# Kernel tuning notes

Hardware: AMD Instinct MI355X
Metric: run time of the kernel (lower is better)

Reference implementation:

```python
import jax, jax.numpy as jnp
import numpy as np

ENCODER_STRIDE = 320
TEMPERATURE = 1.0


def setup_inputs() -> dict:
    key = jax.random.key(0)
    k1, k2, k3, k4 = jax.random.split(key, 4)
    B, D, T, K = 8, 512, 4096, 4096
    student_features = jax.random.normal(k1, (B, D, T), dtype=jnp.float32)
    codebook = jax.random.normal(k2, (K, D), dtype=jnp.float32)
    teacher_codes = jax.random.randint(k3, (B, T), 0, K, dtype=jnp.int64)
    lengths = jax.random.randint(k4, (B,), 0, T * ENCODER_STRIDE, dtype=jnp.int64)
    return {
        "student_features": student_features,
        "codebook": codebook,
        "teacher_codes": teacher_codes,
        "lengths": lengths,
    }


def reference(student_features, codebook, teacher_codes, lengths):
    B, D, T = student_features.shape
    # length mask over frames: frame t is valid if its start sample < length
    frame_starts = jnp.arange(T, dtype=jnp.int64) * ENCODER_STRIDE  # [T]
    mask = (frame_starts[None, :] < lengths[:, None]).astype(student_features.dtype)  # [B,T]

    z = jnp.transpose(student_features, (0, 2, 1)).reshape(-1, D)  # [N,D], N=B*T

    # cdist p=2: sqrt(|z|^2 + |c|^2 - 2 z.c)
    z2 = jnp.sum(z * z, axis=1, keepdims=True)            # [N,1]
    c2 = jnp.sum(codebook * codebook, axis=1)[None, :]    # [1,K]
    d2 = z2 + c2 - 2.0 * (z @ codebook.T)                 # [N,K]
    dists = jnp.sqrt(jnp.maximum(d2, 1e-12))

    soft_weights = jax.nn.softmax(-dists / TEMPERATURE, axis=1)  # [N,K]
    soft_recon = soft_weights @ codebook                          # [N,D]

    codes_flat = teacher_codes.reshape(-1)                        # [N]
    target_embeddings = jax.lax.stop_gradient(codebook[codes_flat])  # [N,D]

    diff_sq = jnp.mean((soft_recon - target_embeddings) ** 2, axis=1).reshape(B, T)
    loss = jnp.sum(diff_sq * mask) / (jnp.sum(mask) + 1e-8)
    return loss
```

## Files before the change

### kernel.cpp

```cpp
#include <hip/hip_runtime.h>
#include <hip/hip_bf16.h>


#define BB 8
#define DD 512
#define TT 4096
#define KKK 4096
#define ENC_STRIDE 320
#define KT 32
#define NKT (KKK / KT)
#define NW 8
#define ROWS 128
#define KBROW 2056
#define KBBYTES 4112
#define BUFB (8 * KBBYTES)

typedef __attribute__((ext_vector_type(8))) short bf16x8;
typedef __attribute__((ext_vector_type(4))) float f32x4;

union FragU { bf16x8 v; uint2 h2[2]; ushort us[8]; unsigned long long q[2]; uint4 u4; };

static __device__ __forceinline__ ushort f2bf(float x) {
  unsigned u = __float_as_uint(x);
  unsigned r = (u + 0x7FFFu + ((u >> 16) & 1u)) >> 16;
  return (ushort)r;
}
static __device__ __forceinline__ uint2 f4tobf(float4 v) {
  uint2 r;
  r.x = (unsigned)f2bf(v.x) | ((unsigned)f2bf(v.y) << 16);
  r.y = (unsigned)f2bf(v.z) | ((unsigned)f2bf(v.w) << 16);
  return r;
}
static __device__ __forceinline__ void gld_lds16(const void* g, void* l) {
  __builtin_amdgcn_global_load_lds(
      (const __attribute__((address_space(1))) unsigned*)g,
      (__attribute__((address_space(3))) unsigned*)l, 16, 0, 0);
}
static __device__ __forceinline__ unsigned lds_addr(const void* p) {
  return (unsigned)(size_t)(const __attribute__((address_space(3))) char*)p;
}

__global__ __launch_bounds__(256) void vq_prep(const float* __restrict__ cb,
                                               float* __restrict__ c2,
                                               ushort* __restrict__ cbh) {
  int k = blockIdx.x * 4 + (threadIdx.x >> 6);
  int lane = threadIdx.x & 63;
  const float4* p = (const float4*)(cb + (size_t)k * DD + lane * 8);
  float4 a = p[0], b = p[1];
  if (cbh) {
    uint2 pa = f4tobf(a), pb = f4tobf(b);
    *(uint4*)(cbh + (size_t)k * DD + lane * 8) = make_uint4(pa.x, pa.y, pb.x, pb.y);
  }
  float s = a.x*a.x + a.y*a.y + a.z*a.z + a.w*a.w
          + b.x*b.x + b.y*b.y + b.z*b.z + b.w*b.w;
  #pragma unroll
  for (int m = 1; m <= 32; m <<= 1) s += __shfl_xor(s, m);
  if (lane == 0) c2[k] = s;
}

template <int GLD>
__global__ __launch_bounds__(512, 2) void vq_main(
    const float* __restrict__ sf,
    const float* __restrict__ cb,
    const ushort* __restrict__ cbh,
    const int*  __restrict__ codes,
    const int*  __restrict__ lens,
    const float* __restrict__ c2,
    float* __restrict__ num) {
  __shared__ __align__(128) ushort cs[4][8][KBROW];
  __shared__ ushort wlds[2][NW][16][36];
  __shared__ float  alds[2][ROWS];
  __shared__ float  llds[ROWS];
  __shared__ float  diffred[ROWS];
  __shared__ int    flagv[NKT];

  const int bid = blockIdx.x;
  const int b  = bid >> 5;
  const int t0 = (bid & 31) << 7;
  const int len = lens[b];
  int vcount = (len + (ENC_STRIDE - 1)) / ENC_STRIDE;
  vcount = vcount < TT ? vcount : TT;
  if (t0 >= vcount) return;

  const int tid = threadIdx.x;
  const int w  = tid >> 6;
  const int l  = tid & 63;
  const int lg = l >> 4;
  const int ln = l & 15;

  for (int i = tid; i < ROWS; i += 512) diffred[i] = 0.f;
  for (int i = tid; i < NKT; i += 512) flagv[i] = 0;

  const float* sfb = sf + (size_t)b * DD * TT;
  const int trow = t0 + w * 16 + ln;
  bf16x8 za[16];
  float z2 = 0.f;
  #pragma unroll
  for (int f = 0; f < 16; ++f) {
    #pragma unroll
    for (int j = 0; j < 8; ++j) {
      int d = f * 32 + lg * 8 + j;
      float v = sfb[(size_t)d * TT + trow];
      z2 += v * v;
      za[f][j] = (short)f2bf(v);
    }
  }
  z2 += __shfl_xor(z2, 16);
  z2 += __shfl_xor(z2, 32);

  const int sbase = (w * 4 + ((l >> 1) & 3)) * DD + (l >> 3) * 16 + (l & 1) * 8;

  auto stage = [&](int kt, int buf) {
    if (GLD) {
      const ushort* gb = cbh + (size_t)kt * KT * DD + sbase;
      ushort* lb = &cs[buf][w][0];
      #pragma unroll
      for (int q = 0; q < 4; ++q) gld_lds16(gb + q * 128, lb + q * 512);
    } else {
      const float* gb = cb + (size_t)kt * KT * DD + sbase;
      #pragma unroll
      for (int q = 0; q < 4; ++q) {
        float4 v0 = *(const float4*)(gb + q * 128);
        float4 v1 = *(const float4*)(gb + q * 128 + 4);
        uint2 a0 = f4tobf(v0), a1 = f4tobf(v1);
        *(uint4*)&cs[buf][w][q * 512 + l * 8] = make_uint4(a0.x, a0.y, a1.x, a1.y);
      }
    }
  };

  stage(0, 0); stage(1, 1); stage(2, 2);

  float mrow = -1e30f, lrow = 0.f;
  f32x4 acc[8][4];
  #pragma unroll
  for (int r = 0; r < 8; ++r)
    #pragma unroll
    for (int nt = 0; nt < 4; ++nt) acc[r][nt] = (f32x4){0.f, 0.f, 0.f, 0.f};

  const unsigned score_lane = (unsigned)((ln >> 2) * KBBYTES + (ln & 3) * 32
                                         + (lg >> 1) * 128 + (lg & 1) * 16);
  const unsigned tr_lane = (unsigned)(lg * KBBYTES + w * 512 + ln * 8);
  const unsigned cs0a = lds_addr(&cs[0][0][0]);

  auto scores_softmax = [&](int it, int sbuf) {
    const char* csb = (const char*)&cs[sbuf][0][0];
    f32x4 sc0 = (f32x4){0,0,0,0}, sc1 = (f32x4){0,0,0,0};
    #pragma unroll
    for (int f = 0; f < 16; ++f) {
      bf16x8 a0 = *(const bf16x8*)(csb + score_lane + f * 256);
      bf16x8 a1 = *(const bf16x8*)(csb + score_lane + 16448 + f * 256);
      sc0 = __builtin_amdgcn_mfma_f32_16x16x32_bf16(a0, za[f], sc0, 0, 0, 0);
      sc1 = __builtin_amdgcn_mfma_f32_16x16x32_bf16(a1, za[f], sc1, 0, 0, 0);
    }
    const float4 c2a = *(const float4*)(c2 + it * KT + lg * 4);
    const float4 c2b = *(const float4*)(c2 + it * KT + 16 + lg * 4);
    float sv[8];
    float c2v[8] = {c2a.x, c2a.y, c2a.z, c2a.w, c2b.x, c2b.y, c2b.z, c2b.w};
    #pragma unroll
    for (int v = 0; v < 4; ++v) {
      sv[v]     = -sqrtf(fmaxf(z2 + c2v[v]     - 2.f * sc0[v], 1e-12f));
      sv[4 + v] = -sqrtf(fmaxf(z2 + c2v[4 + v] - 2.f * sc1[v], 1e-12f));
    }
    float tmax = sv[0];
    #pragma unroll
    for (int i = 1; i < 8; ++i) tmax = fmaxf(tmax, sv[i]);
    tmax = fmaxf(tmax, __shfl_xor(tmax, 16));
    tmax = fmaxf(tmax, __shfl_xor(tmax, 32));
    const bool defer = (tmax <= mrow + 8.f);
    const float mnew = defer ? mrow : tmax;
    float e[8], esum = 0.f;
    #pragma unroll
    for (int i = 0; i < 8; ++i) { e[i] = __expf(sv[i] - mnew); esum += e[i]; }
    esum += __shfl_xor(esum, 16);
    esum += __shfl_xor(esum, 32);
    const float alpha = defer ? 1.f : __expf(mrow - mnew);
    lrow = lrow * alpha + esum;
    mrow = mnew;
    const int s = it & 1;
    uint2 lopk, hipk;
    lopk.x = (unsigned)f2bf(e[0]) | ((unsigned)f2bf(e[1]) << 16);
    lopk.y = (unsigned)f2bf(e[2]) | ((unsigned)f2bf(e[3]) << 16);
    hipk.x = (unsigned)f2bf(e[4]) | ((unsigned)f2bf(e[5]) << 16);
    hipk.y = (unsigned)f2bf(e[6]) | ((unsigned)f2bf(e[7]) << 16);
    *(uint2*)&wlds[s][w][ln][lg * 4]      = lopk;
    *(uint2*)&wlds[s][w][ln][16 + lg * 4] = hipk;
    if (lg == 0) alds[s][w * 16 + ln] = alpha;
    if (!__all(defer) && l == 0) flagv[it] = 1;
  };

  auto recon = [&](int itm1) {
    const int s = itm1 & 1;
    const int rb = itm1 & 3;
    const unsigned trb = cs0a + (unsigned)rb * BUFB + tr_lane;
    unsigned long long tq0[4], tq1[4];
    #pragma unroll
    for (int nt = 0; nt < 4; ++nt) {
      asm volatile("ds_read_b64_tr_b16 %0, %2 offset:%3\n\t"
                   "ds_read_b64_tr_b16 %1, %2 offset:%4"
                   : "=&v"(tq0[nt]), "=&v"(tq1[nt])
                   : "v"(trb), "i"(nt * 128), "i"(16448 + nt * 128));
    }
    asm volatile("s_waitcnt lgkmcnt(0)" ::: "memory");
    __builtin_amdgcn_sched_barrier(0);
    FragU cf[4];
    #pragma unroll
    for (int nt = 0; nt < 4; ++nt) { cf[nt].q[0] = tq0[nt]; cf[nt].q[1] = tq1[nt]; }
    if (flagv[itm1]) {
      #pragma unroll
      for (int r = 0; r < 8; ++r)
        #pragma unroll
        for (int v = 0; v < 4; ++v) {
          float av = alds[s][r * 16 + lg * 4 + v];
          #pragma unroll
          for (int nt = 0; nt < 4; ++nt) acc[r][nt][v] *= av;
        }
    }
    #pragma unroll
    for (int rh = 0; rh < 2; ++rh) {
      FragU wa[4];
      #pragma unroll
      for (int r4 = 0; r4 < 4; ++r4) {
        wa[r4].h2[0] = *(const uint2*)&wlds[s][rh * 4 + r4][ln][lg * 4];
        wa[r4].h2[1] = *(const uint2*)&wlds[s][rh * 4 + r4][ln][16 + lg * 4];
      }
      #pragma unroll
      for (int r4 = 0; r4 < 4; ++r4)
        #pragma unroll
        for (int nt = 0; nt < 4; ++nt)
          acc[rh * 4 + r4][nt] = __builtin_amdgcn_mfma_f32_16x16x32_bf16(
              wa[r4].v, cf[nt].v, acc[rh * 4 + r4][nt], 0, 0, 0);
    }
  };

  __syncthreads();
  scores_softmax(0, 0);

  #pragma unroll 1
  for (int it = 1; it < NKT; ++it) {
    __syncthreads();
    if (it + 2 < NKT) stage(it + 2, (it + 2) & 3);
    recon(it - 1);
    scores_softmax(it, it & 3);
  }
  __syncthreads();
  recon(NKT - 1);

  if (lg == 0) llds[w * 16 + ln] = lrow;
  __syncthreads();
  const int* tcodes = codes + b * TT + t0;
  #pragma unroll
  for (int r = 0; r < 8; ++r) {
    float pv[4];
    #pragma unroll
    for (int v = 0; v < 4; ++v) {
      const int row = r * 16 + lg * 4 + v;
      const float lv = llds[row];
      const int tc = tcodes[row];
      const float* erow = cb + (size_t)tc * DD + w * 64;
      float ps = 0.f;
      #pragma unroll
      for (int nt = 0; nt < 4; ++nt) {
        float rc = acc[r][nt][v] / lv;
        float df = rc - erow[nt * 16 + ln];
        ps += df * df;
      }
      pv[v] = ps;
    }
    #pragma unroll
    for (int v = 0; v < 4; ++v) {
      pv[v] += __shfl_xor(pv[v], 1);
      pv[v] += __shfl_xor(pv[v], 2);
      pv[v] += __shfl_xor(pv[v], 4);
      pv[v] += __shfl_xor(pv[v], 8);
    }
    if (ln == 0) {
      #pragma unroll
      for (int v = 0; v < 4; ++v)
        atomicAdd(&diffred[r * 16 + lg * 4 + v], pv[v]);
    }
  }
  __syncthreads();
  if (tid < ROWS) {
    float val = (t0 + tid < vcount) ? diffred[tid] * (1.f / DD) : 0.f;
    val += __shfl_xor(val, 1);
    val += __shfl_xor(val, 2);
    val += __shfl_xor(val, 4);
    val += __shfl_xor(val, 8);
    val += __shfl_xor(val, 16);
    val += __shfl_xor(val, 32);
    if ((tid & 63) == 0) atomicAdd(num, val);
  }
}

__global__ void vq_finalize(const float* __restrict__ num,
                            const int* __restrict__ lens,
                            float* __restrict__ out) {
  float denom = 0.f;
  for (int b = 0; b < BB; ++b) {
    int v = (lens[b] + (ENC_STRIDE - 1)) / ENC_STRIDE;
    v = v < TT ? v : TT;
    denom += (float)v;
  }
  out[0] = num[0] / (denom + 1e-8f);
}

extern "C" void kernel_launch(void* const* d_in, const int* in_sizes, int n_in,
                              void* d_out, int out_size, void* d_ws, size_t ws_size,
                              hipStream_t stream) {
  const float* sf    = (const float*)d_in[0];
  const float* cb    = (const float*)d_in[1];
  const int*   codes = (const int*)d_in[2];
  const int*   lens  = (const int*)d_in[3];
  float* out = (float*)d_out;
  float* num = (float*)d_ws;
  float* c2  = (float*)((char*)d_ws + 256);
  const size_t need = 32768 + (size_t)KKK * DD * sizeof(ushort);
  ushort* cbh = (ws_size >= need) ? (ushort*)((char*)d_ws + 32768) : nullptr;

  hipMemsetAsync(d_ws, 0, 4, stream);
  vq_prep<<<KKK / 4, 256, 0, stream>>>(cb, c2, cbh);
  const int grid = (BB * TT) / ROWS;
  if (cbh)
    vq_main<1><<<grid, 512, 0, stream>>>(sf, cb, cbh, codes, lens, c2, num);
  else
    vq_main<0><<<grid, 512, 0, stream>>>(sf, cb, cbh, codes, lens, c2, num);
  vq_finalize<<<1, 1, 0, stream>>>(num, lens, out);
}
```

Measured before the change: 366.8 us.

## Reorder loop so score MFMAs overlap softmax and recon with priority hints

The fused loop body is restructured. Each iteration now issues the score MFMAs for the current tile first, then loads all recon operands (transposed codebook reads and softmax weights) in one batch, then computes the softmax while those loads are in flight, and finally runs the recon MFMAs. s_setprio is raised around the MFMA blocks. Softmax exponentials are computed against a per-lane max and rescaled by one factor, and bf16 packing switches from round-to-nearest to truncation. Costs are higher register pressure from holding eight weight fragments and slightly lower precision from truncating to bf16.

```diff
diff --git a/kernel.cpp b/kernel.cpp
--- a/kernel.cpp
+++ b/kernel.cpp
@@ -30,6 +30,9 @@
   r.x = (unsigned)f2bf(v.x) | ((unsigned)f2bf(v.y) << 16);
   r.y = (unsigned)f2bf(v.z) | ((unsigned)f2bf(v.w) << 16);
   return r;
+}
+static __device__ __forceinline__ unsigned pk2bf(float lo, float hi) {
+  return (__float_as_uint(lo) >> 16) | (__float_as_uint(hi) & 0xFFFF0000u);
 }
 static __device__ __forceinline__ void gld_lds16(const void* g, void* l) {
   __builtin_amdgcn_global_load_lds(
@@ -109,7 +112,6 @@
   z2 += __shfl_xor(z2, 32);
 
   const int sbase = (w * 4 + ((l >> 1) & 3)) * DD + (l >> 3) * 16 + (l & 1) * 8;
-
   auto stage = [&](int kt, int buf) {
     if (GLD) {
       const ushort* gb = cbh + (size_t)kt * KT * DD + sbase;
@@ -142,9 +144,11 @@
   const unsigned tr_lane = (unsigned)(lg * KBBYTES + w * 512 + ln * 8);
   const unsigned cs0a = lds_addr(&cs[0][0][0]);
 
-  auto scores_softmax = [&](int it, int sbuf) {
+  f32x4 sc0, sc1;
+  auto scores = [&](int it, int sbuf) {
     const char* csb = (const char*)&cs[sbuf][0][0];
-    f32x4 sc0 = (f32x4){0,0,0,0}, sc1 = (f32x4){0,0,0,0};
+    sc0 = (f32x4){0,0,0,0}; sc1 = (f32x4){0,0,0,0};
+    __builtin_amdgcn_s_setprio(1);
     #pragma unroll
     for (int f = 0; f < 16; ++f) {
       bf16x8 a0 = *(const bf16x8*)(csb + score_lane + f * 256);
@@ -152,46 +156,55 @@
       sc0 = __builtin_amdgcn_mfma_f32_16x16x32_bf16(a0, za[f], sc0, 0, 0, 0);
       sc1 = __builtin_amdgcn_mfma_f32_16x16x32_bf16(a1, za[f], sc1, 0, 0, 0);
     }
-    const float4 c2a = *(const float4*)(c2 + it * KT + lg * 4);
-    const float4 c2b = *(const float4*)(c2 + it * KT + 16 + lg * 4);
+    __builtin_amdgcn_s_setprio(0);
+  };
+
+  __syncthreads();
+  scores(0, 0);
+  {
+    const float4 c2a = *(const float4*)(c2 + lg * 4);
+    const float4 c2b = *(const float4*)(c2 + 16 + lg * 4);
+    float c2v[8] = {c2a.x, c2a.y, c2a.z, c2a.w, c2b.x, c2b.y, c2b.z, c2b.w};
     float sv[8];
-    float c2v[8] = {c2a.x, c2a.y, c2a.z, c2a.w, c2b.x, c2b.y, c2b.z, c2b.w};
     #pragma unroll
     for (int v = 0; v < 4; ++v) {
       sv[v]     = -sqrtf(fmaxf(z2 + c2v[v]     - 2.f * sc0[v], 1e-12f));
       sv[4 + v] = -sqrtf(fmaxf(z2 + c2v[4 + v] - 2.f * sc1[v], 1e-12f));
     }
-    float tmax = sv[0];
-    #pragma unroll
-    for (int i = 1; i < 8; ++i) tmax = fmaxf(tmax, sv[i]);
-    tmax = fmaxf(tmax, __shfl_xor(tmax, 16));
+    float lmax = sv[0];
+    #pragma unroll
+    for (int i = 1; i < 8; ++i) lmax = fmaxf(lmax, sv[i]);
+    float tmax = fmaxf(lmax, __shfl_xor(lmax, 16));
     tmax = fmaxf(tmax, __shfl_xor(tmax, 32));
-    const bool defer = (tmax <= mrow + 8.f);
-    const float mnew = defer ? mrow : tmax;
-    float e[8], esum = 0.f;
-    #pragma unroll
-    for (int i = 0; i < 8; ++i) { e[i] = __expf(sv[i] - mnew); esum += e[i]; }
+    float el[8], lsum = 0.f;
+    #pragma unroll
+    for (int i = 0; i < 8; ++i) { el[i] = __expf(sv[i] - lmax); lsum += el[i]; }
+    mrow = tmax;
+    float factor = __expf(lmax - tmax);
+    float esum = lsum * factor;
     esum += __shfl_xor(esum, 16);
     esum += __shfl_xor(esum, 32);
-    const float alpha = defer ? 1.f : __expf(mrow - mnew);
-    lrow = lrow * alpha + esum;
-    mrow = mnew;
-    const int s = it & 1;
+    lrow = esum;
     uint2 lopk, hipk;
-    lopk.x = (unsigned)f2bf(e[0]) | ((unsigned)f2bf(e[1]) << 16);
-    lopk.y = (unsigned)f2bf(e[2]) | ((unsigned)f2bf(e[3]) << 16);
-    hipk.x = (unsigned)f2bf(e[4]) | ((unsigned)f2bf(e[5]) << 16);
-    hipk.y = (unsigned)f2bf(e[6]) | ((unsigned)f2bf(e[7]) << 16);
-    *(uint2*)&wlds[s][w][ln][lg * 4]      = lopk;
-    *(uint2*)&wlds[s][w][ln][16 + lg * 4] = hipk;
-    if (lg == 0) alds[s][w * 16 + ln] = alpha;
-    if (!__all(defer) && l == 0) flagv[it] = 1;
-  };
-
-  auto recon = [&](int itm1) {
+    lopk.x = pk2bf(el[0] * factor, el[1] * factor);
+    lopk.y = pk2bf(el[2] * factor, el[3] * factor);
+    hipk.x = pk2bf(el[4] * factor, el[5] * factor);
+    hipk.y = pk2bf(el[6] * factor, el[7] * factor);
+    *(uint2*)&wlds[0][w][ln][lg * 4]      = lopk;
+    *(uint2*)&wlds[0][w][ln][16 + lg * 4] = hipk;
+    if (lg == 0) alds[0][w * 16 + ln] = 1.f;
+  }
+
+  #pragma unroll 1
+  for (int it = 1; it < NKT; ++it) {
+    __syncthreads();
+    if (it + 2 < NKT) stage(it + 2, (it + 2) & 3);
+
+    scores(it, it & 3);
+
+    const int itm1 = it - 1;
     const int s = itm1 & 1;
-    const int rb = itm1 & 3;
-    const unsigned trb = cs0a + (unsigned)rb * BUFB + tr_lane;
+    const unsigned trb = cs0a + (unsigned)(itm1 & 3) * BUFB + tr_lane;
     unsigned long long tq0[4], tq1[4];
     #pragma unroll
     for (int nt = 0; nt < 4; ++nt) {
@@ -200,12 +213,17 @@
                    : "=&v"(tq0[nt]), "=&v"(tq1[nt])
                    : "v"(trb), "i"(nt * 128), "i"(16448 + nt * 128));
     }
+    FragU wa[8];
+    #pragma unroll
+    for (int r = 0; r < 8; ++r) {
+      wa[r].h2[0] = *(const uint2*)&wlds[s][r][ln][lg * 4];
+      wa[r].h2[1] = *(const uint2*)&wlds[s][r][ln][16 + lg * 4];
+    }
+    const int flg = flagv[itm1];
     asm volatile("s_waitcnt lgkmcnt(0)" ::: "memory");
     __builtin_amdgcn_sched_barrier(0);
-    FragU cf[4];
-    #pragma unroll
-    for (int nt = 0; nt < 4; ++nt) { cf[nt].q[0] = tq0[nt]; cf[nt].q[1] = tq1[nt]; }
-    if (flagv[itm1]) {
+
+    if (flg) {
       #pragma unroll
       for (int r = 0; r < 8; ++r)
         #pragma unroll
@@ -215,35 +233,100 @@
           for (int nt = 0; nt < 4; ++nt) acc[r][nt][v] *= av;
         }
     }
-    #pragma unroll
-    for (int rh = 0; rh < 2; ++rh) {
-      FragU wa[4];
-      #pragma unroll
-      for (int r4 = 0; r4 < 4; ++r4) {
-        wa[r4].h2[0] = *(const uint2*)&wlds[s][rh * 4 + r4][ln][lg * 4];
-        wa[r4].h2[1] = *(const uint2*)&wlds[s][rh * 4 + r4][ln][16 + lg * 4];
-      }
-      #pragma unroll
-      for (int r4 = 0; r4 < 4; ++r4)
+
+    FragU cf[4];
+    #pragma unroll
+    for (int nt = 0; nt < 4; ++nt) { cf[nt].q[0] = tq0[nt]; cf[nt].q[1] = tq1[nt]; }
+
+    const float4 c2a = *(const float4*)(c2 + it * KT + lg * 4);
+    const float4 c2b = *(const float4*)(c2 + it * KT + 16 + lg * 4);
+    float c2v[8] = {c2a.x, c2a.y, c2a.z, c2a.w, c2b.x, c2b.y, c2b.z, c2b.w};
+    float sv[8];
+    #pragma unroll
+    for (int v = 0; v < 4; ++v) {
+      sv[v]     = -sqrtf(fmaxf(z2 + c2v[v]     - 2.f * sc0[v], 1e-12f));
+      sv[4 + v] = -sqrtf(fmaxf(z2 + c2v[4 + v] - 2.f * sc1[v], 1e-12f));
+    }
+    float lmax = sv[0];
+    #pragma unroll
+    for (int i = 1; i < 8; ++i) lmax = fmaxf(lmax, sv[i]);
+    float tmax = fmaxf(lmax, __shfl_xor(lmax, 16));
+    tmax = fmaxf(tmax, __shfl_xor(tmax, 32));
+    float el[8], lsum = 0.f;
+    #pragma unroll
+    for (int i = 0; i < 8; ++i) { el[i] = __expf(sv[i] - lmax); lsum += el[i]; }
+    const bool defer = (tmax <= mrow + 8.f);
+    const float mnew = defer ? mrow : tmax;
+    const float factor = __expf(lmax - mnew);
+    float esum = lsum * factor;
+    esum += __shfl_xor(esum, 16);
+    esum += __shfl_xor(esum, 32);
+    const float alpha = defer ? 1.f : __expf(mrow - mnew);
+    lrow = lrow * alpha + esum;
+    mrow = mnew;
+    uint2 lopk, hipk;
+    lopk.x = pk2bf(el[0] * factor, el[1] * factor);
+    lopk.y = pk2bf(el[2] * factor, el[3] * factor);
+    hipk.x = pk2bf(el[4] * factor, el[5] * factor);
+    hipk.y = pk2bf(el[6] * factor, el[7] * factor);
+    const int s2 = it & 1;
+    *(uint2*)&wlds[s2][w][ln][lg * 4]      = lopk;
+    *(uint2*)&wlds[s2][w][ln][16 + lg * 4] = hipk;
+    if (lg == 0) alds[s2][w * 16 + ln] = alpha;
+    if (!__all(defer) && l == 0) flagv[it] = 1;
+
+    __builtin_amdgcn_s_setprio(1);
+    #pragma unroll
+    for (int r = 0; r < 8; ++r)
+      #pragma unroll
+      for (int nt = 0; nt < 4; ++nt)
+        acc[r][nt] = __builtin_amdgcn_mfma_f32_16x16x32_bf16(
+            wa[r].v, cf[nt].v, acc[r][nt], 0, 0, 0);
+    __builtin_amdgcn_s_setprio(0);
+  }
+
+  __syncthreads();
+  {
+    const int itm1 = NKT - 1;
+    const int s = itm1 & 1;
+    const unsigned trb = cs0a + (unsigned)(itm1 & 3) * BUFB + tr_lane;
+    unsigned long long tq0[4], tq1[4];
+    #pragma unroll
+    for (int nt = 0; nt < 4; ++nt) {
+      asm volatile("ds_read_b64_tr_b16 %0, %2 offset:%3\n\t"
+                   "ds_read_b64_tr_b16 %1, %2 offset:%4"
+                   : "=&v"(tq0[nt]), "=&v"(tq1[nt])
+                   : "v"(trb), "i"(nt * 128), "i"(16448 + nt * 128));
+    }
+    FragU wa[8];
+    #pragma unroll
+    for (int r = 0; r < 8; ++r) {
+      wa[r].h2[0] = *(const uint2*)&wlds[s][r][ln][lg * 4];
+      wa[r].h2[1] = *(const uint2*)&wlds[s][r][ln][16 + lg * 4];
+    }
+    const int flg = flagv[itm1];
+    asm volatile("s_waitcnt lgkmcnt(0)" ::: "memory");
+    __builtin_amdgcn_sched_barrier(0);
+    if (flg) {
+      #pragma unroll
+      for (int r = 0; r < 8; ++r)
         #pragma unroll
-        for (int nt = 0; nt < 4; ++nt)
-          acc[rh * 4 + r4][nt] = __builtin_amdgcn_mfma_f32_16x16x32_bf16(
-              wa[r4].v, cf[nt].v, acc[rh * 4 + r4][nt], 0, 0, 0);
-    }
-  };
-
-  __syncthreads();
-  scores_softmax(0, 0);
-
-  #pragma unroll 1
-  for (int it = 1; it < NKT; ++it) {
-    __syncthreads();
-    if (it + 2 < NKT) stage(it + 2, (it + 2) & 3);
-    recon(it - 1);
-    scores_softmax(it, it & 3);
-  }
-  __syncthreads();
-  recon(NKT - 1);
+        for (int v = 0; v < 4; ++v) {
+          float av = alds[s][r * 16 + lg * 4 + v];
+          #pragma unroll
+          for (int nt = 0; nt < 4; ++nt) acc[r][nt][v] *= av;
+        }
+    }
+    FragU cf[4];
+    #pragma unroll
+    for (int nt = 0; nt < 4; ++nt) { cf[nt].q[0] = tq0[nt]; cf[nt].q[1] = tq1[nt]; }
+    #pragma unroll
+    for (int r = 0; r < 8; ++r)
+      #pragma unroll
+      for (int nt = 0; nt < 4; ++nt)
+        acc[r][nt] = __builtin_amdgcn_mfma_f32_16x16x32_bf16(
+            wa[r].v, cf[nt].v, acc[r][nt], 0, 0, 0);
+  }
 
   if (lg == 0) llds[w * 16 + ln] = lrow;
   __syncthreads();
```

New measurement: 1.143 ms. +211.5%, slower.
